# Kernel tuning notes

Measured on AMD Instinct MI355X. Metric: run time of the kernel, lower is better.

The kernel has to match this reference:

```python
import jax, jax.numpy as jnp
import numpy as np

HIDDEN = 512
HEADS = 8
HEAD_DIM = HIDDEN // HEADS   # 64
MAN_DIM = 256                # manifold_dim = hidden_dim // 2
SCALE = HEAD_DIM ** -0.5


def _c(re, im):
    return jax.lax.complex(re, im)


def setup_inputs() -> dict:
    key = jax.random.key(0)
    ks = jax.random.split(key, 13)
    def w(k, shape, fan_in):
        return (jax.random.normal(k, shape, dtype=jnp.float32) / np.sqrt(fan_in)).astype(jnp.float32)
    B, S = 2, 2048
    return {
        "x": jax.random.normal(ks[0], (B, S, HIDDEN), dtype=jnp.float32),
        "Wq_re": w(ks[1], (HIDDEN, HIDDEN), HIDDEN), "Wq_im": w(ks[2], (HIDDEN, HIDDEN), HIDDEN),
        "Wk_re": w(ks[3], (HIDDEN, HIDDEN), HIDDEN), "Wk_im": w(ks[4], (HIDDEN, HIDDEN), HIDDEN),
        "Wv_re": w(ks[5], (HIDDEN, HIDDEN), HIDDEN), "Wv_im": w(ks[6], (HIDDEN, HIDDEN), HIDDEN),
        "Wm_re": w(ks[7], (HEAD_DIM, MAN_DIM), HEAD_DIM), "Wm_im": w(ks[8], (HEAD_DIM, MAN_DIM), HEAD_DIM),
        "Wmi_re": w(ks[9], (MAN_DIM, HEAD_DIM), MAN_DIM), "Wmi_im": w(ks[10], (MAN_DIM, HEAD_DIM), MAN_DIM),
        "Wo_re": w(ks[11], (HIDDEN, HIDDEN), HIDDEN), "Wo_im": w(ks[12], (HIDDEN, HIDDEN), HIDDEN),
    }


def reference(x, Wq_re, Wq_im, Wk_re, Wk_im, Wv_re, Wv_im,
              Wm_re, Wm_im, Wmi_re, Wmi_im, Wo_re, Wo_im):
    B, S, D = x.shape
    # quantum state preparation: cast to complex, L2-normalize along last dim
    xc = x.astype(jnp.complex64)
    norm = jnp.linalg.norm(xc, axis=-1, keepdims=True)
    xc = xc / norm

    Wq, Wk, Wv = _c(Wq_re, Wq_im), _c(Wk_re, Wk_im), _c(Wv_re, Wv_im)
    Wm, Wmi, Wo = _c(Wm_re, Wm_im), _c(Wmi_re, Wmi_im), _c(Wo_re, Wo_im)

    def heads(t):  # [B,S,D] -> [B,H,S,head_dim]
        return t.reshape(B, S, HEADS, HEAD_DIM).transpose(0, 2, 1, 3)

    q = heads(xc @ Wq)
    k = heads(xc @ Wk)
    v = heads(xc @ Wv)

    # project each head onto the manifold (complex linear)
    qm = jnp.einsum('bhsd,dm->bhsm', q, Wm)
    km = jnp.einsum('bhsd,dm->bhsm', k, Wm)
    vm = jnp.einsum('bhsd,dm->bhsm', v, Wm)

    # Hermitian inner product attention scores; softmax over real part
    scores = jnp.einsum('bhqm,bhkm->bhqk', qm, jnp.conj(km)) * SCALE
    attn = jax.nn.softmax(scores.real, axis=-1).astype(jnp.complex64)

    outm = jnp.einsum('bhqk,bhkm->bhqm', attn, vm)
    out = jnp.einsum('bhsm,md->bhsd', outm, Wmi)        # back to head_dim
    out = out.transpose(0, 2, 1, 3).reshape(B, S, D)    # merge heads
    out = out @ Wo
    # return real/imag stacked as float32 (complex64 output -> [B,S,D,2])
    return jnp.stack([out.real, out.imag], axis=-1)
```

## Files before the change

### kernel.cpp

```cpp
#include <hip/hip_runtime.h>
#include <hip/hip_bf16.h>
#include <stdint.h>


typedef __attribute__((ext_vector_type(8))) short bf16x8;
typedef __attribute__((ext_vector_type(4))) float f32x4;

#define QSCALE 0.18033688011112042f

__device__ __forceinline__ unsigned short f2b(float f) {
    union { float f; unsigned int u; } v; v.f = f;
    unsigned int r = v.u + 0x7fffu + ((v.u >> 16) & 1u);
    return (unsigned short)(r >> 16);
}

__device__ __forceinline__ float b2f(short s) {
    union { float f; unsigned int u; } v;
    v.u = ((unsigned int)(unsigned short)s) << 16;
    return v.f;
}

__device__ __forceinline__ unsigned int cvtpk(float a, float b) {
    union { __hip_bfloat162 h; unsigned int u; } v;
    v.h = __float22bfloat162_rn(make_float2(a, b));
    return v.u;
}

__device__ __forceinline__ void ld16(void* lds, const void* g) {
    __builtin_amdgcn_global_load_lds(
        (__attribute__((address_space(1))) unsigned int*)(g),
        (__attribute__((address_space(3))) unsigned int*)(lds), 16, 0, 0);
}

__global__ __launch_bounds__(256) void k_prep(
        const float* __restrict__ x, unsigned short* __restrict__ xn,
        const float* __restrict__ s0, const float* __restrict__ s1,
        const float* __restrict__ s2, const float* __restrict__ s3,
        const float* __restrict__ s4, const float* __restrict__ s5,
        const float* __restrict__ s6, const float* __restrict__ s7,
        float* __restrict__ d0, float* __restrict__ d1,
        float* __restrict__ d2, float* __restrict__ d3,
        float* __restrict__ d4, float* __restrict__ d5,
        float* __restrict__ d6, float* __restrict__ d7) {
    __shared__ float tile[64][65];
    if (blockIdx.x < 1024) {
        int row  = blockIdx.x * 4 + (threadIdx.x >> 6);
        int lane = threadIdx.x & 63;
        const float4* xr = (const float4*)(x + (size_t)row * 512);
        float4 a = xr[lane], b = xr[lane + 64];
        float s = a.x*a.x + a.y*a.y + a.z*a.z + a.w*a.w
                + b.x*b.x + b.y*b.y + b.z*b.z + b.w*b.w;
        #pragma unroll
        for (int m = 1; m < 64; m <<= 1) s += __shfl_xor(s, m, 64);
        float inv = 1.0f / sqrtf(s);
        ushort4 o;
        o.x = f2b(a.x*inv); o.y = f2b(a.y*inv); o.z = f2b(a.z*inv); o.w = f2b(a.w*inv);
        *(ushort4*)&xn[(size_t)row*512 + lane*4] = o;
        o.x = f2b(b.x*inv); o.y = f2b(b.y*inv); o.z = f2b(b.z*inv); o.w = f2b(b.w*inv);
        *(ushort4*)&xn[(size_t)row*512 + 256 + lane*4] = o;
        return;
    }
    int bid = blockIdx.x - 1024;
    const float* src; float* dst; int R, C, tr, tc;
    if (bid < 384) {
        int mat = bid >> 6, tl = bid & 63;
        src = (mat==0)?s0:(mat==1)?s1:(mat==2)?s2:(mat==3)?s3:(mat==4)?s4:s5;
        dst = (mat==0)?d0:(mat==1)?d1:(mat==2)?d2:(mat==3)?d3:(mat==4)?d4:d5;
        R = 512; C = 512; tr = tl >> 3; tc = tl & 7;
    } else {
        int mat = (bid - 384) >> 2, tl = (bid - 384) & 3;
        src = mat ? s7 : s6; dst = mat ? d7 : d6;
        R = 64; C = 256; tr = 0; tc = tl;
    }
    int r0 = tr * 64, c0 = tc * 64;
    int tx = threadIdx.x & 63, ty = threadIdx.x >> 6;
    #pragma unroll
    for (int i = 0; i < 16; i++) {
        int r = ty + i*4;
        tile[r][tx] = src[(size_t)(r0 + r)*C + c0 + tx];
    }
    __syncthreads();
    #pragma unroll
    for (int i = 0; i < 16; i++) {
        int r = ty + i*4;
        dst[(size_t)(c0 + r)*R + r0 + tx] = tile[tx][r];
    }
}

__global__ __launch_bounds__(256) void k_gh(const float* __restrict__ Wm_re, const float* __restrict__ Wm_im,
                                            const float* __restrict__ WmT_re, const float* __restrict__ WmT_im,
                                            const float* __restrict__ Wmi_re, const float* __restrict__ Wmi_im,
                                            float* __restrict__ GH) {
    int id = blockIdx.x * 256 + threadIdx.x;
    int mat = id >> 12;
    int a = (id >> 6) & 63, c = id & 63;
    float s = 0.f;
    if (mat < 2) {
        for (int m = 0; m < 256; m++) {
            float ar = Wm_re[a*256+m], ai = Wm_im[a*256+m];
            float br = WmT_re[m*64+c], bi = WmT_im[m*64+c];
            s += (mat == 0) ? (ar*br + ai*bi) : (ai*br - ar*bi);
        }
        GH[id] = s;
    } else {
        for (int m = 0; m < 256; m++) {
            float ar = Wm_re[a*256+m], ai = Wm_im[a*256+m];
            float br = Wmi_re[m*64+c], bi = Wmi_im[m*64+c];
            s += (mat == 2) ? (ar*br - ai*bi) : (ar*bi + ai*br);
        }
        GH[mat*4096 + c*64 + a] = s;
    }
}

__global__ __launch_bounds__(256) void k_pack(
        const float* __restrict__ WqT_re, const float* __restrict__ WqT_im,
        const float* __restrict__ WkT_re, const float* __restrict__ WkT_im,
        const float* __restrict__ WvT_re, const float* __restrict__ WvT_im,
        const float* __restrict__ Wo_re,  const float* __restrict__ Wo_im,
        const float* __restrict__ GH,
        unsigned short* __restrict__ WqkvT, unsigned short* __restrict__ Wbig) {
    if (blockIdx.x < 6144) {
        int id = blockIdx.x * 256 + threadIdx.x;
        int n = id >> 9, k = id & 511;
        float val;
        if (n < 1024) {
            int h = n >> 7, part = (n >> 6) & 1, j = n & 63;
            const float* Gr = GH;
            const float* Gi = GH + 4096;
            const float* qr = WqT_re + (size_t)(h*64)*512 + k;
            const float* qi = WqT_im + (size_t)(h*64)*512 + k;
            float s = 0.f;
            if (part == 0) { for (int d = 0; d < 64; d++) s += qr[d*512]*Gr[d*64+j] - qi[d*512]*Gi[d*64+j]; }
            else           { for (int d = 0; d < 64; d++) s += qr[d*512]*Gi[d*64+j] + qi[d*512]*Gr[d*64+j]; }
            val = s * QSCALE;
        } else if (n < 2048) {
            int m = n - 1024; int h = m >> 7, part = (m >> 6) & 1, j = m & 63;
            val = (part ? WkT_im : WkT_re)[(size_t)(h*64+j)*512 + k];
        } else {
            int m = n - 2048; int h = m >> 7, part = (m >> 6) & 1, j = m & 63;
            val = (part ? WvT_im : WvT_re)[(size_t)(h*64+j)*512 + k];
        }
        WqkvT[id] = f2b(val);
    } else {
        int id = (blockIdx.x - 6144) * 256 + threadIdx.x;
        int np = id >> 10, kk = id & 1023;
        int c = np >> 1, p = np & 1;
        int h = kk >> 7, pp = (kk >> 6) & 1, d = kk & 63;
        const float* HrT = GH + 2*4096;
        const float* HiT = GH + 3*4096;
        float s = 0.f;
        if (p == pp) {
            for (int j = 0; j < 64; j++) {
                float hr = HrT[j*64+d], hi = HiT[j*64+d];
                float wr = Wo_re[(size_t)(h*64+j)*512 + c];
                float wi = Wo_im[(size_t)(h*64+j)*512 + c];
                s += hr*wr - hi*wi;
            }
        } else {
            for (int j = 0; j < 64; j++) {
                float hr = HrT[j*64+d], hi = HiT[j*64+d];
                float wr = Wo_re[(size_t)(h*64+j)*512 + c];
                float wi = Wo_im[(size_t)(h*64+j)*512 + c];
                s += hr*wi + hi*wr;
            }
            if (p == 0) s = -s;
        }
        Wbig[(size_t)np*1024 + kk] = f2b(s);
    }
}

template<int MODE, int MT>
__global__ __launch_bounds__(256, 2) void k_gemm(
        const unsigned short* __restrict__ Ain, const unsigned short* __restrict__ Btin,
        void* __restrict__ Cout, unsigned short* __restrict__ Vt,
        const float* __restrict__ Lp, int K) {
    __shared__ __align__(16) unsigned short Al[2][MT*32];
    __shared__ __align__(16) unsigned short Bl[2][128*32];
    const int t = threadIdx.x;
    const int wave = t >> 6, lane = t & 63, quad = lane >> 4, l16 = lane & 15;
    const int wr = wave >> 1, wc = wave & 1;

    const unsigned short* A;
    const unsigned short* Bt;
    unsigned short* Cb = nullptr;
    int m0, n0;
    if (MODE == 0) {
        if (blockIdx.y < 16) {
            A = Ain; Bt = Btin;
            m0 = blockIdx.x * 128; n0 = blockIdx.y * 128;
            Cb = (unsigned short*)Cout;
        } else {
            int idx = (blockIdx.y - 16) * 32 + blockIdx.x;
            int b = idx >> 7, mt = (idx >> 4) & 7, nt = idx & 15;
            A  = Btin + 2048*512;
            Bt = Ain + (size_t)b*2048*512;
            m0 = mt * 128; n0 = nt * 128;
            Cb = Vt + (size_t)b*1024*2048;
        }
    } else {
        A = Ain; Bt = Btin;
        m0 = blockIdx.x * MT; n0 = blockIdx.y * 128;
    }

    f32x4 acc[MT/32][4] = {};
    for (int kt = 0; kt < K; kt += 64) {
        if (MODE == 1) {
            int r = t >> 2, gr = t & 3;
            int row = m0 + r;
            #pragma unroll
            for (int kh = 0; kh < 2; kh++) {
                int kk = kt + kh*32 + gr*8;
                int hh = kk >> 7;
                float l0 = Lp[(size_t)row*8 + hh];
                float l1 = Lp[32768 + (size_t)row*8 + hh];
                float invl = 1.0f / (l0 + l1);
                float w0 = l0*invl, w1 = l1*invl;
                size_t off = (size_t)row*1024 + kk;
                bf16x8 a0 = *(const bf16x8*)&Ain[off];
                bf16x8 a1 = *(const bf16x8*)&Ain[4194304 + off];
                uint4 u;
                u.x = cvtpk(w0*b2f(a0[0]) + w1*b2f(a1[0]), w0*b2f(a0[1]) + w1*b2f(a1[1]));
                u.y = cvtpk(w0*b2f(a0[2]) + w1*b2f(a1[2]), w0*b2f(a0[3]) + w1*b2f(a1[3]));
                u.z = cvtpk(w0*b2f(a0[4]) + w1*b2f(a1[4]), w0*b2f(a0[5]) + w1*b2f(a1[5]));
                u.w = cvtpk(w0*b2f(a0[6]) + w1*b2f(a1[6]), w0*b2f(a0[7]) + w1*b2f(a1[7]));
                *(uint4*)&Al[kh][t*8] = u;
            }
        } else {
            #pragma unroll
            for (int kh = 0; kh < 2; kh++)
                #pragma unroll
                for (int i = 0; i < MT/64; i++) {
                    int g = t + i*256, r = g >> 2, gr = g & 3;
                    ld16(&Al[kh][g*8], &A[(size_t)(m0 + r)*K + kt + kh*32 + gr*8]);
                }
        }
        #pragma unroll
        for (int kh = 0; kh < 2; kh++)
            #pragma unroll
            for (int i = 0; i < 2; i++) {
                int g = t + i*256, r = g >> 2, gr = g & 3;
                ld16(&Bl[kh][g*8], &Bt[(size_t)(n0 + r)*K + kt + kh*32 + gr*8]);
            }
        __syncthreads();
        #pragma unroll
        for (int kh = 0; kh < 2; kh++) {
            bf16x8 af[MT/32], bfr[4];
            #pragma unroll
            for (int rt = 0; rt < MT/32; rt++)
                af[rt] = *(const bf16x8*)&Al[kh][(wr*(MT/2) + rt*16 + l16)*32 + quad*8];
            #pragma unroll
            for (int ct = 0; ct < 4; ct++)
                bfr[ct] = *(const bf16x8*)&Bl[kh][(wc*64 + ct*16 + l16)*32 + quad*8];
            #pragma unroll
            for (int rt = 0; rt < MT/32; rt++)
                #pragma unroll
                for (int ct = 0; ct < 4; ct++)
                    acc[rt][ct] = __builtin_amdgcn_mfma_f32_16x16x32_bf16(af[rt], bfr[ct], acc[rt][ct], 0, 0, 0);
        }
        __syncthreads();
    }
    #pragma unroll
    for (int rt = 0; rt < MT/32; rt++) {
        int row = m0 + wr*(MT/2) + rt*16 + quad*4;
        #pragma unroll
        for (int ct = 0; ct < 4; ct++) {
            int col = n0 + wc*64 + ct*16 + l16;
            if (MODE == 0) {
                unsigned int u01 = cvtpk(acc[rt][ct][0], acc[rt][ct][1]);
                unsigned int u23 = cvtpk(acc[rt][ct][2], acc[rt][ct][3]);
                Cb[(size_t)(row+0)*2048 + col] = (unsigned short)(u01);
                Cb[(size_t)(row+1)*2048 + col] = (unsigned short)(u01 >> 16);
                Cb[(size_t)(row+2)*2048 + col] = (unsigned short)(u23);
                Cb[(size_t)(row+3)*2048 + col] = (unsigned short)(u23 >> 16);
            } else {
                float* C = (float*)Cout;
                #pragma unroll
                for (int r = 0; r < 4; r++)
                    C[(size_t)(row + r)*1024 + col] = acc[rt][ct][r];
            }
        }
    }
}

__global__ __launch_bounds__(256, 2) void k_attn(
        const unsigned short* __restrict__ QK,
        const unsigned short* __restrict__ Vt,
        unsigned short* __restrict__ Opart,
        float* __restrict__ Lpart) {
    __shared__ __align__(16) unsigned short Kl[2][8192];
    __shared__ __align__(16) unsigned short Vl[2][8192];
    __shared__ __align__(16) unsigned short Pl[4608];

    const int t = threadIdx.x, w = t >> 6, lane = t & 63, quad = lane >> 4, l16 = lane & 15;
    const int bh = blockIdx.x, b = bh >> 3, h = bh & 7;
    const int qb = blockIdx.y & 15, half = blockIdx.y >> 4;
    const int tok0 = b*2048 + qb*128;

    bf16x8 qf[2][4];
    #pragma unroll
    for (int rt = 0; rt < 2; rt++)
        #pragma unroll
        for (int ks = 0; ks < 4; ks++)
            qf[rt][ks] = *(const bf16x8*)&QK[(size_t)(tok0 + w*32 + rt*16 + l16)*2048 + h*128 + ks*32 + quad*8];

    const unsigned short* kp = QK + (size_t)(b*2048 + half*1024 + (t >> 2))*2048 + 1024 + h*128 + (t & 3)*8;
    const unsigned short* vp = Vt + (size_t)(b*1024 + h*128 + (t >> 2))*2048 + half*1024 + (t & 3)*8;

    f32x4 Oacc[2][8] = {};
    float ls[2][4] = {};

    #pragma unroll
    for (int i = 0; i < 4; i++) ld16(&Kl[0][(i*256 + t)*8], kp + i*32);
    #pragma unroll
    for (int i = 0; i < 4; i++) ld16(&Vl[0][(i*256 + t)*8], vp + (i & 1)*131072 + (i >> 1)*32);
    __syncthreads();

    for (int it = 0; it < 16; it++) {
        const int cur = it & 1;
        if (it < 15) {
            int kt2 = (it + 1) * 64;
            #pragma unroll
            for (int i = 0; i < 4; i++) ld16(&Kl[cur^1][(i*256 + t)*8], kp + (size_t)kt2*2048 + i*32);
            #pragma unroll
            for (int i = 0; i < 4; i++) ld16(&Vl[cur^1][(i*256 + t)*8], vp + kt2 + (i & 1)*131072 + (i >> 1)*32);
        }

        f32x4 S[2][4] = {};
        #pragma unroll
        for (int ks = 0; ks < 4; ks++) {
            #pragma unroll
            for (int ct = 0; ct < 4; ct++) {
                bf16x8 kf = *(const bf16x8*)&Kl[cur][ks*2048 + (ct*16 + l16)*32 + quad*8];
                #pragma unroll
                for (int rt = 0; rt < 2; rt++)
                    S[rt][ct] = __builtin_amdgcn_mfma_f32_16x16x32_bf16(qf[rt][ks], kf, S[rt][ct], 0, 0, 0);
            }
        }
        #pragma unroll
        for (int ks2 = 0; ks2 < 2; ks2++) {
            #pragma unroll
            for (int rt = 0; rt < 2; rt++) {
                #pragma unroll
                for (int ct2 = 0; ct2 < 2; ct2++) {
                    int ct = ks2*2 + ct2;
                    float p0 = exp2f(S[rt][ct][0]), p1 = exp2f(S[rt][ct][1]);
                    float p2 = exp2f(S[rt][ct][2]), p3 = exp2f(S[rt][ct][3]);
                    ls[rt][0] += p0; ls[rt][1] += p1; ls[rt][2] += p2; ls[rt][3] += p3;
                    int q = w*32 + rt*16 + quad*4;
                    int base = ct2*16 + l16;
                    unsigned int u01 = cvtpk(p0, p1);
                    unsigned int u23 = cvtpk(p2, p3);
                    Pl[base + (q+0)*36] = (unsigned short)(u01);
                    Pl[base + (q+1)*36] = (unsigned short)(u01 >> 16);
                    Pl[base + (q+2)*36] = (unsigned short)(u23);
                    Pl[base + (q+3)*36] = (unsigned short)(u23 >> 16);
                }
            }
            bf16x8 pf[2];
            #pragma unroll
            for (int rt = 0; rt < 2; rt++)
                pf[rt] = *(const bf16x8*)&Pl[(w*32 + rt*16 + l16)*36 + quad*8];
            #pragma unroll
            for (int dt = 0; dt < 8; dt++) {
                bf16x8 vf = *(const bf16x8*)&Vl[cur][ks2*4096 + (dt*16 + l16)*32 + quad*8];
                #pragma unroll
                for (int rt = 0; rt < 2; rt++)
                    Oacc[rt][dt] = __builtin_amdgcn_mfma_f32_16x16x32_bf16(pf[rt], vf, Oacc[rt][dt], 0, 0, 0);
            }
        }
        __syncthreads();
    }

    #pragma unroll
    for (int rt = 0; rt < 2; rt++)
        #pragma unroll
        for (int r = 0; r < 4; r++) {
            float s = ls[rt][r];
            #pragma unroll
            for (int m = 1; m < 16; m <<= 1) s += __shfl_xor(s, m, 64);
            ls[rt][r] = s;
        }
    unsigned short* Op = Opart + (size_t)half*4096*1024;
    float* Lp = Lpart + (size_t)half*32768;
    #pragma unroll
    for (int rt = 0; rt < 2; rt++) {
        int q = w*32 + rt*16 + quad*4;
        int tok = tok0 + q;
        float inv[4];
        #pragma unroll
        for (int r = 0; r < 4; r++) inv[r] = 1.0f / ls[rt][r];
        if (l16 == 0) {
            #pragma unroll
            for (int r = 0; r < 4; r++) Lp[(size_t)(tok + r)*8 + h] = ls[rt][r];
        }
        #pragma unroll
        for (int dt = 0; dt < 8; dt++) {
            int col = h*128 + dt*16 + l16;
            #pragma unroll
            for (int r = 0; r < 4; r++)
                Op[(size_t)(tok + r)*1024 + col] = f2b(Oacc[rt][dt][r] * inv[r]);
        }
    }
}

extern "C" void kernel_launch(void* const* d_in, const int* in_sizes, int n_in,
                              void* d_out, int out_size, void* d_ws, size_t ws_size,
                              hipStream_t stream) {
    (void)in_sizes; (void)n_in; (void)out_size; (void)ws_size;
    const float* x      = (const float*)d_in[0];
    const float* Wq_re  = (const float*)d_in[1];
    const float* Wq_im  = (const float*)d_in[2];
    const float* Wk_re  = (const float*)d_in[3];
    const float* Wk_im  = (const float*)d_in[4];
    const float* Wv_re  = (const float*)d_in[5];
    const float* Wv_im  = (const float*)d_in[6];
    const float* Wm_re  = (const float*)d_in[7];
    const float* Wm_im  = (const float*)d_in[8];
    const float* Wmi_re = (const float*)d_in[9];
    const float* Wmi_im = (const float*)d_in[10];
    const float* Wo_re  = (const float*)d_in[11];
    const float* Wo_im  = (const float*)d_in[12];

    char* ws = (char*)d_ws;
    unsigned short* xn    = (unsigned short*)(ws);
    unsigned short* WqkvT = (unsigned short*)(ws + (4u << 20));
    unsigned short* Wbig  = (unsigned short*)(ws + (7u << 20));
    float*          GH    = (float*)         (ws + (9u << 20));
    float*          WmT_re= (float*)         (ws + (9u << 20) + (64u << 10));
    float*          WmT_im= (float*)         (ws + (9u << 20) + (128u << 10));
    unsigned short* QK    = (unsigned short*)(ws + (10u << 20));
    unsigned short* Vt    = (unsigned short*)(ws + (26u << 20));
    unsigned short* Opart = (unsigned short*)(ws + (42u << 20));
    float*          Lpart = (float*)         (ws + (74u << 20));
    float* WqT_re = (float*)(ws + (10u << 20));
    float* WqT_im = (float*)(ws + (11u << 20));
    float* WkT_re = (float*)(ws + (12u << 20));
    float* WkT_im = (float*)(ws + (13u << 20));
    float* WvT_re = (float*)(ws + (14u << 20));
    float* WvT_im = (float*)(ws + (15u << 20));

    k_prep      <<<dim3(1416), dim3(256), 0, stream>>>(
        x, xn,
        Wq_re, Wq_im, Wk_re, Wk_im, Wv_re, Wv_im, Wm_re, Wm_im,
        WqT_re, WqT_im, WkT_re, WkT_im, WvT_re, WvT_im, WmT_re, WmT_im);
    k_gh        <<<dim3(64),   dim3(256), 0, stream>>>(Wm_re, Wm_im, WmT_re, WmT_im, Wmi_re, Wmi_im, GH);
    k_pack      <<<dim3(10240),dim3(256), 0, stream>>>(
        WqT_re, WqT_im, WkT_re, WkT_im, WvT_re, WvT_im, Wo_re, Wo_im, GH, WqkvT, Wbig);
    k_gemm<0,128><<<dim3(32, 24), dim3(256), 0, stream>>>(xn, WqkvT, (void*)QK, Vt, nullptr, 512);
    k_attn      <<<dim3(16, 32), dim3(256), 0, stream>>>(QK, Vt, Opart, Lpart);
    k_gemm<1,64> <<<dim3(64, 8), dim3(256), 0, stream>>>(Opart, Wbig, d_out, nullptr, Lpart, 1024);
}
```

Before: 246.0 us.

## Fold Wq into manifold Gram via MFMA GEMM, transpose K/V weights directly, swizzle attention LDS

The scalar k_pack loop that multiplied Wq by the manifold Gram matrix for every output element is replaced by a small bf16 MFMA GEMM (new MODE 2 of k_gemm) on a packed Aq/Bq layout. Wk/Wv are transposed straight into the bf16 packed WqkvT inside k_prep, which removes the fp32 intermediate transposes and the later repack pass. The attention kernel also XOR-swizzles its K/V LDS load and read offsets to cut bank conflicts. The risk is that the folded Wq product is now computed from bf16 inputs, which lowers its precision, and the swizzle has to match on both the write and read sides.

Result: faster. 236.9 us (-3.7%).

```diff
diff --git a/kernel.cpp b/kernel.cpp
--- a/kernel.cpp
+++ b/kernel.cpp
@@ -34,14 +34,12 @@
 
 __global__ __launch_bounds__(256) void k_prep(
         const float* __restrict__ x, unsigned short* __restrict__ xn,
-        const float* __restrict__ s0, const float* __restrict__ s1,
-        const float* __restrict__ s2, const float* __restrict__ s3,
-        const float* __restrict__ s4, const float* __restrict__ s5,
-        const float* __restrict__ s6, const float* __restrict__ s7,
-        float* __restrict__ d0, float* __restrict__ d1,
-        float* __restrict__ d2, float* __restrict__ d3,
-        float* __restrict__ d4, float* __restrict__ d5,
-        float* __restrict__ d6, float* __restrict__ d7) {
+        const float* __restrict__ Wq_re, const float* __restrict__ Wq_im,
+        const float* __restrict__ Wk_re, const float* __restrict__ Wk_im,
+        const float* __restrict__ Wv_re, const float* __restrict__ Wv_im,
+        const float* __restrict__ Wm_re, const float* __restrict__ Wm_im,
+        unsigned short* __restrict__ WqkvT, unsigned short* __restrict__ Bq,
+        float* __restrict__ WmT_re, float* __restrict__ WmT_im) {
     __shared__ float tile[64][65];
     if (blockIdx.x < 1024) {
         int row  = blockIdx.x * 4 + (threadIdx.x >> 6);
@@ -61,36 +59,58 @@
         return;
     }
     int bid = blockIdx.x - 1024;
-    const float* src; float* dst; int R, C, tr, tc;
-    if (bid < 384) {
+    int tx = threadIdx.x & 63, ty = threadIdx.x >> 6;
+    if (bid < 256) {
         int mat = bid >> 6, tl = bid & 63;
-        src = (mat==0)?s0:(mat==1)?s1:(mat==2)?s2:(mat==3)?s3:(mat==4)?s4:s5;
-        dst = (mat==0)?d0:(mat==1)?d1:(mat==2)?d2:(mat==3)?d3:(mat==4)?d4:d5;
-        R = 512; C = 512; tr = tl >> 3; tc = tl & 7;
+        const float* src = (mat==0)?Wk_re:(mat==1)?Wk_im:(mat==2)?Wv_re:Wv_im;
+        int r0 = (tl >> 3) * 64, c0 = (tl & 7) * 64;
+        #pragma unroll
+        for (int i = 0; i < 16; i++) {
+            int r = ty + i*4;
+            tile[r][tx] = src[(size_t)(r0 + r)*512 + c0 + tx];
+        }
+        __syncthreads();
+        int sec = 1024 + (mat >> 1)*1024, part = mat & 1;
+        #pragma unroll
+        for (int i = 0; i < 16; i++) {
+            int r = ty + i*4;
+            int rr = c0 + r, h = rr >> 6, j = rr & 63;
+            WqkvT[(size_t)(sec + h*128 + part*64 + j)*512 + r0 + tx] = f2b(tile[tx][r]);
+        }
+    } else if (bid < 264) {
+        int mat = (bid - 256) >> 2, tl = (bid - 256) & 3;
+        const float* src = mat ? Wm_im : Wm_re;
+        float* dst = mat ? WmT_im : WmT_re;
+        int c0 = tl * 64;
+        #pragma unroll
+        for (int i = 0; i < 16; i++) {
+            int r = ty + i*4;
+            tile[r][tx] = src[(size_t)r*256 + c0 + tx];
+        }
+        __syncthreads();
+        #pragma unroll
+        for (int i = 0; i < 16; i++) {
+            int r = ty + i*4;
+            dst[(size_t)(c0 + r)*64 + tx] = tile[tx][r];
+        }
     } else {
-        int mat = (bid - 384) >> 2, tl = (bid - 384) & 3;
-        src = mat ? s7 : s6; dst = mat ? d7 : d6;
-        R = 64; C = 256; tr = 0; tc = tl;
-    }
-    int r0 = tr * 64, c0 = tc * 64;
-    int tx = threadIdx.x & 63, ty = threadIdx.x >> 6;
-    #pragma unroll
-    for (int i = 0; i < 16; i++) {
-        int r = ty + i*4;
-        tile[r][tx] = src[(size_t)(r0 + r)*C + c0 + tx];
-    }
-    __syncthreads();
-    #pragma unroll
-    for (int i = 0; i < 16; i++) {
-        int r = ty + i*4;
-        dst[(size_t)(c0 + r)*R + r0 + tx] = tile[tx][r];
+        int b3 = bid - 264;
+        int mat = b3 >> 6, tl = b3 & 63;
+        const float* src = mat ? Wq_im : Wq_re;
+        #pragma unroll
+        for (int i = 0; i < 16; i++) {
+            int idx = tl*4096 + i*256 + threadIdx.x;
+            int k = idx >> 9, col = idx & 511;
+            int h = col >> 6, d = col & 63;
+            Bq[(size_t)(h*512 + k)*128 + mat*64 + d] = f2b(src[(size_t)k*512 + col]);
+        }
     }
 }
 
 __global__ __launch_bounds__(256) void k_gh(const float* __restrict__ Wm_re, const float* __restrict__ Wm_im,
                                             const float* __restrict__ WmT_re, const float* __restrict__ WmT_im,
                                             const float* __restrict__ Wmi_re, const float* __restrict__ Wmi_im,
-                                            float* __restrict__ GH) {
+                                            float* __restrict__ GH, unsigned short* __restrict__ Aq) {
     int id = blockIdx.x * 256 + threadIdx.x;
     int mat = id >> 12;
     int a = (id >> 6) & 63, c = id & 63;
@@ -101,7 +121,14 @@
             float br = WmT_re[m*64+c], bi = WmT_im[m*64+c];
             s += (mat == 0) ? (ar*br + ai*bi) : (ai*br - ar*bi);
         }
-        GH[id] = s;
+        float sq = s * QSCALE;
+        if (mat == 0) {
+            Aq[c*128 + a]           = f2b(sq);
+            Aq[(64+c)*128 + 64 + a] = f2b(sq);
+        } else {
+            Aq[(64+c)*128 + a]      = f2b(sq);
+            Aq[c*128 + 64 + a]      = f2b(-sq);
+        }
     } else {
         for (int m = 0; m < 256; m++) {
             float ar = Wm_re[a*256+m], ai = Wm_im[a*256+m];
@@ -112,61 +139,33 @@
     }
 }
 
-__global__ __launch_bounds__(256) void k_pack(
-        const float* __restrict__ WqT_re, const float* __restrict__ WqT_im,
-        const float* __restrict__ WkT_re, const float* __restrict__ WkT_im,
-        const float* __restrict__ WvT_re, const float* __restrict__ WvT_im,
+__global__ __launch_bounds__(256) void k_packwo(
         const float* __restrict__ Wo_re,  const float* __restrict__ Wo_im,
-        const float* __restrict__ GH,
-        unsigned short* __restrict__ WqkvT, unsigned short* __restrict__ Wbig) {
-    if (blockIdx.x < 6144) {
-        int id = blockIdx.x * 256 + threadIdx.x;
-        int n = id >> 9, k = id & 511;
-        float val;
-        if (n < 1024) {
-            int h = n >> 7, part = (n >> 6) & 1, j = n & 63;
-            const float* Gr = GH;
-            const float* Gi = GH + 4096;
-            const float* qr = WqT_re + (size_t)(h*64)*512 + k;
-            const float* qi = WqT_im + (size_t)(h*64)*512 + k;
-            float s = 0.f;
-            if (part == 0) { for (int d = 0; d < 64; d++) s += qr[d*512]*Gr[d*64+j] - qi[d*512]*Gi[d*64+j]; }
-            else           { for (int d = 0; d < 64; d++) s += qr[d*512]*Gi[d*64+j] + qi[d*512]*Gr[d*64+j]; }
-            val = s * QSCALE;
-        } else if (n < 2048) {
-            int m = n - 1024; int h = m >> 7, part = (m >> 6) & 1, j = m & 63;
-            val = (part ? WkT_im : WkT_re)[(size_t)(h*64+j)*512 + k];
-        } else {
-            int m = n - 2048; int h = m >> 7, part = (m >> 6) & 1, j = m & 63;
-            val = (part ? WvT_im : WvT_re)[(size_t)(h*64+j)*512 + k];
-        }
-        WqkvT[id] = f2b(val);
+        const float* __restrict__ GH, unsigned short* __restrict__ Wbig) {
+    int id = blockIdx.x * 256 + threadIdx.x;
+    int np = id >> 10, kk = id & 1023;
+    int c = np >> 1, p = np & 1;
+    int h = kk >> 7, pp = (kk >> 6) & 1, d = kk & 63;
+    const float* HrT = GH + 2*4096;
+    const float* HiT = GH + 3*4096;
+    float s = 0.f;
+    if (p == pp) {
+        for (int j = 0; j < 64; j++) {
+            float hr = HrT[j*64+d], hi = HiT[j*64+d];
+            float wr = Wo_re[(size_t)(h*64+j)*512 + c];
+            float wi = Wo_im[(size_t)(h*64+j)*512 + c];
+            s += hr*wr - hi*wi;
+        }
     } else {
-        int id = (blockIdx.x - 6144) * 256 + threadIdx.x;
-        int np = id >> 10, kk = id & 1023;
-        int c = np >> 1, p = np & 1;
-        int h = kk >> 7, pp = (kk >> 6) & 1, d = kk & 63;
-        const float* HrT = GH + 2*4096;
-        const float* HiT = GH + 3*4096;
-        float s = 0.f;
-        if (p == pp) {
-            for (int j = 0; j < 64; j++) {
-                float hr = HrT[j*64+d], hi = HiT[j*64+d];
-                float wr = Wo_re[(size_t)(h*64+j)*512 + c];
-                float wi = Wo_im[(size_t)(h*64+j)*512 + c];
-                s += hr*wr - hi*wi;
-            }
-        } else {
-            for (int j = 0; j < 64; j++) {
-                float hr = HrT[j*64+d], hi = HiT[j*64+d];
-                float wr = Wo_re[(size_t)(h*64+j)*512 + c];
-                float wi = Wo_im[(size_t)(h*64+j)*512 + c];
-                s += hr*wi + hi*wr;
-            }
-            if (p == 0) s = -s;
-        }
-        Wbig[(size_t)np*1024 + kk] = f2b(s);
-    }
+        for (int j = 0; j < 64; j++) {
+            float hr = HrT[j*64+d], hi = HiT[j*64+d];
+            float wr = Wo_re[(size_t)(h*64+j)*512 + c];
+            float wi = Wo_im[(size_t)(h*64+j)*512 + c];
+            s += hr*wi + hi*wr;
+        }
+        if (p == 0) s = -s;
+    }
+    Wbig[(size_t)np*1024 + kk] = f2b(s);
 }
 
 template<int MODE, int MT>
@@ -272,6 +271,15 @@
                 Cb[(size_t)(row+1)*2048 + col] = (unsigned short)(u01 >> 16);
                 Cb[(size_t)(row+2)*2048 + col] = (unsigned short)(u23);
                 Cb[(size_t)(row+3)*2048 + col] = (unsigned short)(u23 >> 16);
+            } else if (MODE == 2) {
+                unsigned short* Cq = (unsigned short*)Cout;
+                int h = col >> 9, k = col & 511;
+                unsigned int u01 = cvtpk(acc[rt][ct][0], acc[rt][ct][1]);
+                unsigned int u23 = cvtpk(acc[rt][ct][2], acc[rt][ct][3]);
+                Cq[(size_t)(h*128 + row + 0)*512 + k] = (unsigned short)(u01);
+                Cq[(size_t)(h*128 + row + 1)*512 + k] = (unsigned short)(u01 >> 16);
+                Cq[(size_t)(h*128 + row + 2)*512 + k] = (unsigned short)(u23);
+                Cq[(size_t)(h*128 + row + 3)*512 + k] = (unsigned short)(u23 >> 16);
             } else {
                 float* C = (float*)Cout;
                 #pragma unroll
@@ -292,6 +300,7 @@
     __shared__ __align__(16) unsigned short Pl[4608];
 
     const int t = threadIdx.x, w = t >> 6, lane = t & 63, quad = lane >> 4, l16 = lane & 15;
+    const int quadx = quad ^ ((l16 >> 2) & 3);
     const int bh = blockIdx.x, b = bh >> 3, h = bh & 7;
     const int qb = blockIdx.y & 15, half = blockIdx.y >> 4;
     const int tok0 = b*2048 + qb*128;
@@ -303,8 +312,9 @@
         for (int ks = 0; ks < 4; ks++)
             qf[rt][ks] = *(const bf16x8*)&QK[(size_t)(tok0 + w*32 + rt*16 + l16)*2048 + h*128 + ks*32 + quad*8];
 
-    const unsigned short* kp = QK + (size_t)(b*2048 + half*1024 + (t >> 2))*2048 + 1024 + h*128 + (t & 3)*8;
-    const unsigned short* vp = Vt + (size_t)(b*1024 + h*128 + (t >> 2))*2048 + half*1024 + (t & 3)*8;
+    const int grs = (t & 3) ^ ((t >> 4) & 3);
+    const unsigned short* kp = QK + (size_t)(b*2048 + half*1024 + (t >> 2))*2048 + 1024 + h*128 + grs*8;
+    const unsigned short* vp = Vt + (size_t)(b*1024 + h*128 + (t >> 2))*2048 + half*1024 + grs*8;
 
     f32x4 Oacc[2][8] = {};
     float ls[2][4] = {};
@@ -330,7 +340,7 @@
         for (int ks = 0; ks < 4; ks++) {
             #pragma unroll
             for (int ct = 0; ct < 4; ct++) {
-                bf16x8 kf = *(const bf16x8*)&Kl[cur][ks*2048 + (ct*16 + l16)*32 + quad*8];
+                bf16x8 kf = *(const bf16x8*)&Kl[cur][ks*2048 + (ct*16 + l16)*32 + quadx*8];
                 #pragma unroll
                 for (int rt = 0; rt < 2; rt++)
                     S[rt][ct] = __builtin_amdgcn_mfma_f32_16x16x32_bf16(qf[rt][ks], kf, S[rt][ct], 0, 0, 0);
@@ -362,7 +372,7 @@
                 pf[rt] = *(const bf16x8*)&Pl[(w*32 + rt*16 + l16)*36 + quad*8];
             #pragma unroll
             for (int dt = 0; dt < 8; dt++) {
-                bf16x8 vf = *(const bf16x8*)&Vl[cur][ks2*4096 + (dt*16 + l16)*32 + quad*8];
+                bf16x8 vf = *(const bf16x8*)&Vl[cur][ks2*4096 + (dt*16 + l16)*32 + quadx*8];
                 #pragma unroll
                 for (int rt = 0; rt < 2; rt++)
                     Oacc[rt][dt] = __builtin_amdgcn_mfma_f32_16x16x32_bf16(pf[rt], vf, Oacc[rt][dt], 0, 0, 0);
@@ -428,25 +438,21 @@
     float*          GH    = (float*)         (ws + (9u << 20));
     float*          WmT_re= (float*)         (ws + (9u << 20) + (64u << 10));
     float*          WmT_im= (float*)         (ws + (9u << 20) + (128u << 10));
+    unsigned short* Aq    = (unsigned short*)(ws + (9u << 20) + (192u << 10));
     unsigned short* QK    = (unsigned short*)(ws + (10u << 20));
+    unsigned short* Bq    = (unsigned short*)(ws + (10u << 20));
     unsigned short* Vt    = (unsigned short*)(ws + (26u << 20));
     unsigned short* Opart = (unsigned short*)(ws + (42u << 20));
     float*          Lpart = (float*)         (ws + (74u << 20));
-    float* WqT_re = (float*)(ws + (10u << 20));
-    float* WqT_im = (float*)(ws + (11u << 20));
-    float* WkT_re = (float*)(ws + (12u << 20));
-    float* WkT_im = (float*)(ws + (13u << 20));
-    float* WvT_re = (float*)(ws + (14u << 20));
-    float* WvT_im = (float*)(ws + (15u << 20));
-
-    k_prep      <<<dim3(1416), dim3(256), 0, stream>>>(
-        x, xn,
-        Wq_re, Wq_im, Wk_re, Wk_im, Wv_re, Wv_im, Wm_re, Wm_im,
-        WqT_re, WqT_im, WkT_re, WkT_im, WvT_re, WvT_im, WmT_re, WmT_im);
-    k_gh        <<<dim3(64),   dim3(256), 0, stream>>>(Wm_re, Wm_im, WmT_re, WmT_im, Wmi_re, Wmi_im, GH);
-    k_pack      <<<dim3(10240),dim3(256), 0, stream>>>(
-        WqT_re, WqT_im, WkT_re, WkT_im, WvT_re, WvT_im, Wo_re, Wo_im, GH, WqkvT, Wbig);
+
+    k_prep       <<<dim3(1416), dim3(256), 0, stream>>>(
+        x, xn, Wq_re, Wq_im, Wk_re, Wk_im, Wv_re, Wv_im, Wm_re, Wm_im,
+        WqkvT, Bq, WmT_re, WmT_im);
+    k_gh         <<<dim3(64),   dim3(256), 0, stream>>>(
+        Wm_re, Wm_im, WmT_re, WmT_im, Wmi_re, Wmi_im, GH, Aq);
+    k_gemm<2,128><<<dim3(1, 32),  dim3(256), 0, stream>>>(Aq, Bq, (void*)WqkvT, nullptr, nullptr, 128);
+    k_packwo     <<<dim3(4096), dim3(256), 0, stream>>>(Wo_re, Wo_im, GH, Wbig);
     k_gemm<0,128><<<dim3(32, 24), dim3(256), 0, stream>>>(xn, WqkvT, (void*)QK, Vt, nullptr, 512);
-    k_attn      <<<dim3(16, 32), dim3(256), 0, stream>>>(QK, Vt, Opart, Lpart);
-    k_gemm<1,64> <<<dim3(64, 8), dim3(256), 0, stream>>>(Opart, Wbig, d_out, nullptr, Lpart, 1024);
-}
+    k_attn       <<<dim3(16, 32), dim3(256), 0, stream>>>(QK, Vt, Opart, Lpart);
+    k_gemm<1,64> <<<dim3(64, 8),  dim3(256), 0, stream>>>(Opart, Wbig, d_out, nullptr, Lpart, 1024);
+}
```
